# Kernel optimization log

Hardware: AMD Instinct MI355X
Metric: run time of the kernel (lower is better)

## Reference

```python
import math
import jax, jax.numpy as jnp
import numpy as np

NUM_FREQ = 10  # NeRF-style L=10 -> enc dim 3 + 3*2*10 = 63

def pos_encode(coords):
    # freq_bands = 2^i * pi, i = 0..L-1
    freq = (2.0 ** jnp.arange(NUM_FREQ, dtype=coords.dtype)) * math.pi
    scaled = coords[..., None] * freq                      # [E, 3, L]
    enc = jnp.stack([jnp.sin(scaled), jnp.cos(scaled)], axis=-1)  # [E, 3, L, 2]
    enc = enc.reshape(coords.shape[0], -1)                 # [E, 60] interleaved sin/cos
    return jnp.concatenate([coords, enc], axis=-1)         # [E, 63]

def setup_inputs() -> dict:
    key = jax.random.key(0)
    ks = jax.random.split(key, 9)
    N, M, K, C = 65536, 16384, 32, 64
    E = M * K
    x = jax.random.normal(ks[0], (N, C), jnp.float32)
    pos = jax.random.normal(ks[1], (N, 3), jnp.float32)
    batch = jnp.sort(jax.random.randint(ks[2], (N,), 0, 8))
    idx = jax.random.randint(ks[3], (M,), 0, N)
    row = jnp.sort(jax.random.randint(ks[4], (E,), 0, M))
    col = jax.random.randint(ks[5], (E,), 0, N)
    d_in = C + 3 + 3 * 2 * NUM_FREQ  # 127
    def lin(k, i, o):
        s = 1.0 / np.sqrt(i)
        kw, kb = jax.random.split(k)
        return (jax.random.uniform(kw, (i, o), jnp.float32, -s, s),
                jax.random.uniform(kb, (o,), jnp.float32, -s, s))
    lw1, lb1 = lin(ks[6], d_in, 128)
    lw2, lb2 = lin(ks[7], 128, 128)
    gw, gb = lin(ks[8], 128, 256)
    return dict(x=x, pos=pos, batch=batch, idx=idx, row=row, col=col,
                lw1=lw1, lb1=lb1, lw2=lw2, lb2=lb2, gw=gw, gb=gb)

def reference(x, pos, batch, idx, row, col, lw1, lb1, lw2, lb2, gw, gb):
    M = idx.shape[0]
    pos_idx = pos[idx]                         # [M, 3] sampled centers
    pos_diff = pos[col] - pos_idx[row]         # [E, 3] neighbor offsets
    pe = pos_encode(pos_diff)                  # [E, 63]
    edge_in = jnp.concatenate([x[col], pe], axis=-1)   # [E, 127]
    # local_nn: Linear->ReLU->Linear (no final activation, per MLP_Wrapper)
    h = jax.nn.relu(edge_in @ lw1 + lb1)       # [E, 128]
    edge_feat = h @ lw2 + lb2                  # [E, 128]
    # scatter_reduce amax, include_self=False: empty rows stay 0
    agg = jax.ops.segment_max(edge_feat, row, num_segments=M)
    agg = jnp.where(jnp.isneginf(agg), jnp.zeros((), agg.dtype), agg)
    out = agg @ gw + gb                        # [M, 256] global_nn (single Linear)
    return out, pos_idx, batch[idx]
```

## Files before the change

kernel.cpp:

```cpp
#include <hip/hip_runtime.h>
#include <math.h>

#define NN 65536
#define MM 16384
#define EE 524288
#define CF 64
#define HD 128
#define OD 256
#define RPB 8
#define PITCH 129

typedef __bf16 bf16x8 __attribute__((ext_vector_type(8)));
typedef __bf16 bf16x4 __attribute__((ext_vector_type(4)));
typedef float f32x4 __attribute__((ext_vector_type(4)));

__device__ __forceinline__ unsigned enc_f(float f) {
    unsigned u = __float_as_uint(f);
    return (u & 0x80000000u) ? ~u : (u | 0x80000000u);
}
__device__ __forceinline__ float dec_f(unsigned e) {
    unsigned u = (e & 0x80000000u) ? (e ^ 0x80000000u) : ~e;
    return __uint_as_float(u);
}
#define ENC_NEG_INF 0x007FFFFFu

__device__ __forceinline__ unsigned bf_bits(float f) {
    __bf16 b = (__bf16)f;
    return (unsigned)__builtin_bit_cast(unsigned short, b);
}

#define WS_FRAG_OFF 0
#define WS_ROWPTR_OFF 65536
#define WS_XBF_OFF 131072
#define WS_PD_OFF (131072 + 8388608)

__global__ void k_pre(__bf16* __restrict__ fragbuf, int* __restrict__ rowptr,
                      __bf16* __restrict__ xbf, float4* __restrict__ pdbuf,
                      const float* __restrict__ lw1, const float* __restrict__ lw2,
                      const float* __restrict__ x, const int* __restrict__ row,
                      const int* __restrict__ col,
                      const float* __restrict__ pos, const int* __restrict__ batch,
                      const int* __restrict__ idx, float* __restrict__ out) {
    const int b = blockIdx.x;
    const int t = threadIdx.x;
    if (b == 0) {
        const int lane = t & 63;
        const int wv = t >> 6;
        const int q = lane >> 4;
        const int ln = lane & 15;
        #pragma unroll
        for (int fi = 0; fi < 16; ++fi) {
            const int nt = (fi >> 2) & 1, kk = fi & 3;
            const int n = wv * 32 + nt * 16 + ln;
            bf16x8 f;
            #pragma unroll
            for (int j = 0; j < 8; ++j) {
                const int c = kk * 32 + q * 8 + j;
                const int rk = (c < 67) ? c : c - 1;
                f[j] = (fi < 8) ? (__bf16)((c == 67) ? 0.0f : lw1[rk * HD + n])
                                : (__bf16)lw2[c * HD + n];
            }
            *(bf16x8*)&fragbuf[((size_t)fi * 256 + t) * 8] = f;
        }
    } else if (b <= 65) {
        const int i = (b - 1) * 256 + t;
        if (i <= MM) {
            int lo = 0, hi = EE;
            while (lo < hi) { int mid = (lo + hi) >> 1; if (row[mid] < i) lo = mid + 1; else hi = mid; }
            rowptr[i] = lo;
        }
    } else if (b <= 129) {
        const int m = (b - 66) * 256 + t;
        if (m < MM) {
            const int s = idx[m];
            out[MM * OD + m * 3 + 0] = pos[s * 3 + 0];
            out[MM * OD + m * 3 + 1] = pos[s * 3 + 1];
            out[MM * OD + m * 3 + 2] = pos[s * 3 + 2];
            out[MM * OD + MM * 3 + m] = (float)batch[s];
        }
    } else if (b <= 1153) {
        const size_t base = ((size_t)(b - 130) * 256 + t) * 16;
        const float4* xs = (const float4*)(x + base);
        const float4 a = xs[0], c = xs[1], d = xs[2], e = xs[3];
        bf16x8 o0, o1;
        o0[0] = (__bf16)a.x; o0[1] = (__bf16)a.y; o0[2] = (__bf16)a.z; o0[3] = (__bf16)a.w;
        o0[4] = (__bf16)c.x; o0[5] = (__bf16)c.y; o0[6] = (__bf16)c.z; o0[7] = (__bf16)c.w;
        o1[0] = (__bf16)d.x; o1[1] = (__bf16)d.y; o1[2] = (__bf16)d.z; o1[3] = (__bf16)d.w;
        o1[4] = (__bf16)e.x; o1[5] = (__bf16)e.y; o1[6] = (__bf16)e.z; o1[7] = (__bf16)e.w;
        *(bf16x8*)&xbf[base] = o0;
        *(bf16x8*)&xbf[base + 8] = o1;
    } else {
        const int e = (b - 1154) * 256 + t;
        const int r = row[e];
        const int c = col[e];
        const int s = idx[r];
        float4 pd;
        pd.x = pos[c * 3 + 0] - pos[s * 3 + 0];
        pd.y = pos[c * 3 + 1] - pos[s * 3 + 1];
        pd.z = pos[c * 3 + 2] - pos[s * 3 + 2];
        pd.w = 0.0f;
        pdbuf[e] = pd;
    }
}

__launch_bounds__(256)
__global__ void k_fused(const __bf16* __restrict__ xbf, const float4* __restrict__ pdbuf,
                        const int* __restrict__ row, const int* __restrict__ col,
                        const int* __restrict__ rowptr, const __bf16* __restrict__ fragbuf,
                        const float* __restrict__ lb1, const float* __restrict__ lb2,
                        const float* __restrict__ gw, const float* __restrict__ gb,
                        float* __restrict__ out) {
    __shared__ __align__(16) __bf16 einX[64][64];
    __shared__ __align__(16) __bf16 einP[64][64];
    __shared__ __align__(16) __bf16 hbuf[64][HD];
    __shared__ unsigned maxbuf[(RPB + 1) * PITCH];
    __shared__ int srow[2][64];
    const int t = threadIdx.x;
    const int lane = t & 63;
    const int wv = t >> 6;
    const int q = lane >> 4;
    const int ln = lane & 15;
    const int lsw = ln & 7;
    const int m0 = blockIdx.x * RPB;

    const int es = rowptr[m0];
    const int ee = rowptr[m0 + RPB];
    const int ntiles = (ee - es + 63) >> 6;

    for (int i = t; i < (RPB + 1) * PITCH; i += 256) maxbuf[i] = ENC_NEG_INF;

    const int pe_e = t >> 2, pe_part = t & 3, pe_esw = pe_e & 7;
    bf16x8 s0, s1;
    auto issue = [&](int tt) {
        const int eg = min(es + tt * 64 + pe_e, EE - 1);
        const int c = col[eg];
        const bf16x8* xr = (const bf16x8*)(xbf + (size_t)c * CF) + pe_part * 2;
        s0 = xr[0]; s1 = xr[1];
    };
    auto commit = [&]() {
        *(bf16x8*)&einX[pe_e][((pe_part * 2 + 0) ^ pe_esw) * 8] = s0;
        *(bf16x8*)&einX[pe_e][((pe_part * 2 + 1) ^ pe_esw) * 8] = s1;
    };
    auto do_pe = [&](int tt) {
        if (t < 192) {
            const int e = t & 63, d = t >> 6;
            const int sb = tt & 1;
            const int eidx = es + tt * 64 + e;
            const int eg = min(eidx, EE - 1);
            const int esw = e & 7;
            const float4 P = pdbuf[eg];
            const float pd = (d == 0) ? P.x : ((d == 1) ? P.y : P.z);
            if (d == 0) {
                srow[sb][e] = (eidx < ee) ? (row[eg] - m0) : RPB;
                uint2 pkt;
                pkt.x = bf_bits(P.x) | (bf_bits(P.y) << 16);
                pkt.y = bf_bits(P.z);
                *(uint2*)&einP[e][esw * 8] = pkt;
            }
            const float fr = __builtin_amdgcn_fractf(pd * 0.5f);
            float sv = __builtin_amdgcn_sinf(fr);
            float cv = __builtin_amdgcn_cosf(fr);
            #pragma unroll
            for (int l = 0; l < 10; ++l) {
                const int jP = 4 + d * 20 + l * 2;
                *(unsigned*)&einP[e][((jP >> 3) ^ esw) * 8 + (jP & 7)] =
                    bf_bits(sv) | (bf_bits(cv) << 16);
                const float s2 = 2.0f * sv * cv;
                const float c2 = 1.0f - 2.0f * sv * sv;
                sv = s2; cv = c2;
            }
        }
    };

    bf16x8 w1f[2][4];
    #pragma unroll
    for (int nt = 0; nt < 2; ++nt)
        #pragma unroll
        for (int kk = 0; kk < 4; ++kk)
            w1f[nt][kk] = *(const bf16x8*)&fragbuf[((size_t)(nt * 4 + kk) * 256 + t) * 8];
    float4 b1q[2];
    #pragma unroll
    for (int nt = 0; nt < 2; ++nt)
        b1q[nt] = *(const float4*)&lb1[wv * 32 + nt * 16 + q * 4];

    if (ntiles > 0) {
        issue(0);
        commit();
        do_pe(0);
        if (ntiles > 1) issue(1);
    }
    __syncthreads();

    for (int tt = 0; tt < ntiles; ++tt) {
        f32x4 acc[2][4];
        #pragma unroll
        for (int nt = 0; nt < 2; ++nt)
            #pragma unroll
            for (int et = 0; et < 4; ++et)
                acc[nt][et] = (f32x4){b1q[nt].x, b1q[nt].y, b1q[nt].z, b1q[nt].w};
        #pragma unroll
        for (int et = 0; et < 4; ++et) {
            const int e = et * 16 + ln;
            bf16x8 a[4];
            a[0] = *(const bf16x8*)&einX[e][(q ^ lsw) * 8];
            a[1] = *(const bf16x8*)&einX[e][((4 + q) ^ lsw) * 8];
            a[2] = *(const bf16x8*)&einP[e][(q ^ lsw) * 8];
            a[3] = *(const bf16x8*)&einP[e][((4 + q) ^ lsw) * 8];
            #pragma unroll
            for (int kk = 0; kk < 4; ++kk) {
                acc[0][et] = __builtin_amdgcn_mfma_f32_16x16x32_bf16(w1f[0][kk], a[kk], acc[0][et], 0, 0, 0);
                acc[1][et] = __builtin_amdgcn_mfma_f32_16x16x32_bf16(w1f[1][kk], a[kk], acc[1][et], 0, 0, 0);
            }
        }
        #pragma unroll
        for (int et = 0; et < 4; ++et) {
            const int e = et * 16 + ln;
            #pragma unroll
            for (int nt = 0; nt < 2; ++nt) {
                bf16x4 hv;
                hv[0] = (__bf16)fmaxf(acc[nt][et][0], 0.0f);
                hv[1] = (__bf16)fmaxf(acc[nt][et][1], 0.0f);
                hv[2] = (__bf16)fmaxf(acc[nt][et][2], 0.0f);
                hv[3] = (__bf16)fmaxf(acc[nt][et][3], 0.0f);
                const int chunk = wv * 4 + nt * 2 + (q >> 1);
                *(bf16x4*)&hbuf[e][((chunk ^ lsw) * 8) + (q & 1) * 4] = hv;
            }
        }
        __syncthreads();

        {
            if (tt + 1 < ntiles) { commit(); issue(tt + 2 < ntiles ? tt + 2 : tt + 1); }
            bf16x8 w2f[2][4];
            #pragma unroll
            for (int nt = 0; nt < 2; ++nt)
                #pragma unroll
                for (int kk = 0; kk < 4; ++kk)
                    w2f[nt][kk] = *(const bf16x8*)&fragbuf[((size_t)(8 + nt * 4 + kk) * 256 + t) * 8];

            f32x4 acc2[4][2];
            #pragma unroll
            for (int nt = 0; nt < 2; ++nt) {
                const float b2 = lb2[wv * 32 + nt * 16 + ln];
                #pragma unroll
                for (int et = 0; et < 4; ++et)
                    acc2[et][nt] = (f32x4){b2, b2, b2, b2};
            }
            #pragma unroll
            for (int et = 0; et < 4; ++et) {
                const int e = et * 16 + ln;
                #pragma unroll
                for (int kk = 0; kk < 4; ++kk) {
                    bf16x8 ah = *(const bf16x8*)&hbuf[e][((kk * 4 + q) ^ lsw) * 8];
                    acc2[et][0] = __builtin_amdgcn_mfma_f32_16x16x32_bf16(ah, w2f[0][kk], acc2[et][0], 0, 0, 0);
                    acc2[et][1] = __builtin_amdgcn_mfma_f32_16x16x32_bf16(ah, w2f[1][kk], acc2[et][1], 0, 0, 0);
                }
            }
            if (tt + 1 < ntiles) do_pe(tt + 1);
            const int sb = tt & 1;
            #pragma unroll
            for (int et = 0; et < 4; ++et) {
                const int4 R = *(const int4*)&srow[sb][et * 16 + q * 4];
                #pragma unroll
                for (int nt = 0; nt < 2; ++nt) {
                    unsigned* base = maxbuf + (wv * 32 + nt * 16 + ln);
                    const f32x4 vv = acc2[et][nt];
                    int cur = R.x;
                    float m = vv[0];
                    if (R.y != cur) { atomicMax(base + cur * PITCH, enc_f(m)); cur = R.y; m = vv[1]; }
                    else m = fmaxf(m, vv[1]);
                    if (R.z != cur) { atomicMax(base + cur * PITCH, enc_f(m)); cur = R.z; m = vv[2]; }
                    else m = fmaxf(m, vv[2]);
                    if (R.w != cur) { atomicMax(base + cur * PITCH, enc_f(m)); cur = R.w; m = vv[3]; }
                    else m = fmaxf(m, vv[3]);
                    atomicMax(base + cur * PITCH, enc_f(m));
                }
            }
        }
        __syncthreads();
    }

    float* afin = (float*)hbuf;
    for (int i = t; i < RPB * HD; i += 256) {
        const unsigned e = maxbuf[(i >> 7) * PITCH + (i & 127)];
        afin[i] = (e == ENC_NEG_INF) ? 0.0f : dec_f(e);
    }
    __syncthreads();

    const int j4 = (t & 63) * 4;
    const int rbase = (t >> 6) * 2;
    float facc[2][4];
    const float4 bias = *(const float4*)&gb[j4];
    #pragma unroll
    for (int r = 0; r < 2; ++r) { facc[r][0] = bias.x; facc[r][1] = bias.y; facc[r][2] = bias.z; facc[r][3] = bias.w; }
    for (int k = 0; k < 128; k += 4) {
        float4 w0 = *(const float4*)&gw[(k + 0) * OD + j4];
        float4 w1 = *(const float4*)&gw[(k + 1) * OD + j4];
        float4 w2 = *(const float4*)&gw[(k + 2) * OD + j4];
        float4 w3 = *(const float4*)&gw[(k + 3) * OD + j4];
        #pragma unroll
        for (int r = 0; r < 2; ++r) {
            float4 av = *(const float4*)&afin[(rbase + r) * HD + k];
            facc[r][0] += av.x * w0.x + av.y * w1.x + av.z * w2.x + av.w * w3.x;
            facc[r][1] += av.x * w0.y + av.y * w1.y + av.z * w2.y + av.w * w3.y;
            facc[r][2] += av.x * w0.z + av.y * w1.z + av.z * w2.z + av.w * w3.z;
            facc[r][3] += av.x * w0.w + av.y * w1.w + av.z * w2.w + av.w * w3.w;
        }
    }
    #pragma unroll
    for (int r = 0; r < 2; ++r) {
        float4 v; v.x = facc[r][0]; v.y = facc[r][1]; v.z = facc[r][2]; v.w = facc[r][3];
        *(float4*)&out[(size_t)(m0 + rbase + r) * OD + j4] = v;
    }
}

extern "C" void kernel_launch(void* const* d_in, const int* in_sizes, int n_in,
                              void* d_out, int out_size, void* d_ws, size_t ws_size,
                              hipStream_t stream) {
    const float* x   = (const float*)d_in[0];
    const float* pos = (const float*)d_in[1];
    const int* batch = (const int*)d_in[2];
    const int* idx   = (const int*)d_in[3];
    const int* row   = (const int*)d_in[4];
    const int* col   = (const int*)d_in[5];
    const float* lw1 = (const float*)d_in[6];
    const float* lb1 = (const float*)d_in[7];
    const float* lw2 = (const float*)d_in[8];
    const float* lb2 = (const float*)d_in[9];
    const float* gw  = (const float*)d_in[10];
    const float* gb  = (const float*)d_in[11];
    float* out = (float*)d_out;
    __bf16* fragbuf = (__bf16*)((char*)d_ws + WS_FRAG_OFF);
    int* rowptr     = (int*)((char*)d_ws + WS_ROWPTR_OFF);
    __bf16* xbf     = (__bf16*)((char*)d_ws + WS_XBF_OFF);
    float4* pdbuf   = (float4*)((char*)d_ws + WS_PD_OFF);

    hipLaunchKernelGGL(k_pre, dim3(1 + 65 + 64 + 1024 + 2048), dim3(256), 0, stream,
                       fragbuf, rowptr, xbf, pdbuf, lw1, lw2, x, row, col, pos, batch, idx, out);
    hipLaunchKernelGGL(k_fused, dim3(MM / RPB), dim3(256), 0, stream,
                       xbf, pdbuf, row, col, rowptr, fragbuf, lb1, lb2, gw, gb, out);
}
```

Measured before the change: 118.8 us.

## Double edge tile and block size, stream MLP weights per k-slice

Each block now handles 16 output rows and tiles of 128 edges using 512 threads (8 waves). The two halves of the waves each own 64 edges of the tile. The W1/W2 MFMA fragments are no longer held in registers for the whole kernel; they are reloaded from global (L2) per k-slice inside the tile loop, which lowers register pressure to target higher occupancy under launch_bounds(512,4). The intent is to amortize per-block setup, the maxbuf init and the final linear layer over more rows, and to hide latency better. In exchange it adds repeated weight fetches each tile, and the larger shared-memory footprint may cap how many blocks fit per CU.

```diff
diff --git a/kernel.cpp b/kernel.cpp
--- a/kernel.cpp
+++ b/kernel.cpp
@@ -7,7 +7,9 @@
 #define CF 64
 #define HD 128
 #define OD 256
-#define RPB 8
+#define RPB 16
+#define ET 128
+#define BT 512
 #define PITCH 129
 
 typedef __bf16 bf16x8 __attribute__((ext_vector_type(8)));
@@ -103,36 +105,39 @@
     }
 }
 
-__launch_bounds__(256)
+__launch_bounds__(BT, 4)
 __global__ void k_fused(const __bf16* __restrict__ xbf, const float4* __restrict__ pdbuf,
                         const int* __restrict__ row, const int* __restrict__ col,
                         const int* __restrict__ rowptr, const __bf16* __restrict__ fragbuf,
                         const float* __restrict__ lb1, const float* __restrict__ lb2,
                         const float* __restrict__ gw, const float* __restrict__ gb,
                         float* __restrict__ out) {
-    __shared__ __align__(16) __bf16 einX[64][64];
-    __shared__ __align__(16) __bf16 einP[64][64];
-    __shared__ __align__(16) __bf16 hbuf[64][HD];
+    __shared__ __align__(16) __bf16 einX[ET][64];
+    __shared__ __align__(16) __bf16 einP[ET][64];
+    __shared__ __align__(16) __bf16 hbuf[ET][HD];
     __shared__ unsigned maxbuf[(RPB + 1) * PITCH];
-    __shared__ int srow[2][64];
+    __shared__ int srow[2][ET];
     const int t = threadIdx.x;
     const int lane = t & 63;
-    const int wv = t >> 6;
+    const int wv4 = t >> 6;
+    const int hh = wv4 >> 2;
+    const int wv = wv4 & 3;
     const int q = lane >> 4;
     const int ln = lane & 15;
     const int lsw = ln & 7;
+    const int fu = wv * 64 + lane;
     const int m0 = blockIdx.x * RPB;
 
     const int es = rowptr[m0];
     const int ee = rowptr[m0 + RPB];
-    const int ntiles = (ee - es + 63) >> 6;
-
-    for (int i = t; i < (RPB + 1) * PITCH; i += 256) maxbuf[i] = ENC_NEG_INF;
+    const int ntiles = (ee - es + ET - 1) >> 7;
+
+    for (int i = t; i < (RPB + 1) * PITCH; i += BT) maxbuf[i] = ENC_NEG_INF;
 
     const int pe_e = t >> 2, pe_part = t & 3, pe_esw = pe_e & 7;
     bf16x8 s0, s1;
     auto issue = [&](int tt) {
-        const int eg = min(es + tt * 64 + pe_e, EE - 1);
+        const int eg = min(es + tt * ET + pe_e, EE - 1);
         const int c = col[eg];
         const bf16x8* xr = (const bf16x8*)(xbf + (size_t)c * CF) + pe_part * 2;
         s0 = xr[0]; s1 = xr[1];
@@ -142,10 +147,10 @@
         *(bf16x8*)&einX[pe_e][((pe_part * 2 + 1) ^ pe_esw) * 8] = s1;
     };
     auto do_pe = [&](int tt) {
-        if (t < 192) {
-            const int e = t & 63, d = t >> 6;
+        if (t < 384) {
+            const int e = t & 127, d = t >> 7;
             const int sb = tt & 1;
-            const int eidx = es + tt * 64 + e;
+            const int eidx = es + tt * ET + e;
             const int eg = min(eidx, EE - 1);
             const int esw = e & 7;
             const float4 P = pdbuf[eg];
@@ -172,12 +177,6 @@
         }
     };
 
-    bf16x8 w1f[2][4];
-    #pragma unroll
-    for (int nt = 0; nt < 2; ++nt)
-        #pragma unroll
-        for (int kk = 0; kk < 4; ++kk)
-            w1f[nt][kk] = *(const bf16x8*)&fragbuf[((size_t)(nt * 4 + kk) * 256 + t) * 8];
     float4 b1q[2];
     #pragma unroll
     for (int nt = 0; nt < 2; ++nt)
@@ -192,51 +191,46 @@
     __syncthreads();
 
     for (int tt = 0; tt < ntiles; ++tt) {
-        f32x4 acc[2][4];
-        #pragma unroll
-        for (int nt = 0; nt < 2; ++nt)
-            #pragma unroll
-            for (int et = 0; et < 4; ++et)
-                acc[nt][et] = (f32x4){b1q[nt].x, b1q[nt].y, b1q[nt].z, b1q[nt].w};
-        #pragma unroll
-        for (int et = 0; et < 4; ++et) {
-            const int e = et * 16 + ln;
-            bf16x8 a[4];
-            a[0] = *(const bf16x8*)&einX[e][(q ^ lsw) * 8];
-            a[1] = *(const bf16x8*)&einX[e][((4 + q) ^ lsw) * 8];
-            a[2] = *(const bf16x8*)&einP[e][(q ^ lsw) * 8];
-            a[3] = *(const bf16x8*)&einP[e][((4 + q) ^ lsw) * 8];
+        {
+            f32x4 acc[2][4];
+            #pragma unroll
+            for (int nt = 0; nt < 2; ++nt)
+                #pragma unroll
+                for (int et = 0; et < 4; ++et)
+                    acc[nt][et] = (f32x4){b1q[nt].x, b1q[nt].y, b1q[nt].z, b1q[nt].w};
             #pragma unroll
             for (int kk = 0; kk < 4; ++kk) {
-                acc[0][et] = __builtin_amdgcn_mfma_f32_16x16x32_bf16(w1f[0][kk], a[kk], acc[0][et], 0, 0, 0);
-                acc[1][et] = __builtin_amdgcn_mfma_f32_16x16x32_bf16(w1f[1][kk], a[kk], acc[1][et], 0, 0, 0);
-            }
-        }
-        #pragma unroll
-        for (int et = 0; et < 4; ++et) {
-            const int e = et * 16 + ln;
-            #pragma unroll
-            for (int nt = 0; nt < 2; ++nt) {
-                bf16x4 hv;
-                hv[0] = (__bf16)fmaxf(acc[nt][et][0], 0.0f);
-                hv[1] = (__bf16)fmaxf(acc[nt][et][1], 0.0f);
-                hv[2] = (__bf16)fmaxf(acc[nt][et][2], 0.0f);
-                hv[3] = (__bf16)fmaxf(acc[nt][et][3], 0.0f);
-                const int chunk = wv * 4 + nt * 2 + (q >> 1);
-                *(bf16x4*)&hbuf[e][((chunk ^ lsw) * 8) + (q & 1) * 4] = hv;
+                bf16x8 w1a = *(const bf16x8*)&fragbuf[((size_t)(0 * 4 + kk) * 256 + fu) * 8];
+                bf16x8 w1b = *(const bf16x8*)&fragbuf[((size_t)(1 * 4 + kk) * 256 + fu) * 8];
+                #pragma unroll
+                for (int et = 0; et < 4; ++et) {
+                    const int e = hh * 64 + et * 16 + ln;
+                    bf16x8 a = (kk < 2)
+                        ? *(const bf16x8*)&einX[e][((kk * 4 + q) ^ lsw) * 8]
+                        : *(const bf16x8*)&einP[e][(((kk - 2) * 4 + q) ^ lsw) * 8];
+                    acc[0][et] = __builtin_amdgcn_mfma_f32_16x16x32_bf16(w1a, a, acc[0][et], 0, 0, 0);
+                    acc[1][et] = __builtin_amdgcn_mfma_f32_16x16x32_bf16(w1b, a, acc[1][et], 0, 0, 0);
+                }
+            }
+            #pragma unroll
+            for (int et = 0; et < 4; ++et) {
+                const int e = hh * 64 + et * 16 + ln;
+                #pragma unroll
+                for (int nt = 0; nt < 2; ++nt) {
+                    bf16x4 hv;
+                    hv[0] = (__bf16)fmaxf(acc[nt][et][0], 0.0f);
+                    hv[1] = (__bf16)fmaxf(acc[nt][et][1], 0.0f);
+                    hv[2] = (__bf16)fmaxf(acc[nt][et][2], 0.0f);
+                    hv[3] = (__bf16)fmaxf(acc[nt][et][3], 0.0f);
+                    const int chunk = wv * 4 + nt * 2 + (q >> 1);
+                    *(bf16x4*)&hbuf[e][((chunk ^ lsw) * 8) + (q & 1) * 4] = hv;
+                }
             }
         }
         __syncthreads();
 
         {
             if (tt + 1 < ntiles) { commit(); issue(tt + 2 < ntiles ? tt + 2 : tt + 1); }
-            bf16x8 w2f[2][4];
-            #pragma unroll
-            for (int nt = 0; nt < 2; ++nt)
-                #pragma unroll
-                for (int kk = 0; kk < 4; ++kk)
-                    w2f[nt][kk] = *(const bf16x8*)&fragbuf[((size_t)(8 + nt * 4 + kk) * 256 + t) * 8];
-
             f32x4 acc2[4][2];
             #pragma unroll
             for (int nt = 0; nt < 2; ++nt) {
@@ -246,20 +240,22 @@
                     acc2[et][nt] = (f32x4){b2, b2, b2, b2};
             }
             #pragma unroll
-            for (int et = 0; et < 4; ++et) {
-                const int e = et * 16 + ln;
-                #pragma unroll
-                for (int kk = 0; kk < 4; ++kk) {
+            for (int kk = 0; kk < 4; ++kk) {
+                bf16x8 w2a = *(const bf16x8*)&fragbuf[((size_t)(8 + 0 * 4 + kk) * 256 + fu) * 8];
+                bf16x8 w2b = *(const bf16x8*)&fragbuf[((size_t)(8 + 1 * 4 + kk) * 256 + fu) * 8];
+                #pragma unroll
+                for (int et = 0; et < 4; ++et) {
+                    const int e = hh * 64 + et * 16 + ln;
                     bf16x8 ah = *(const bf16x8*)&hbuf[e][((kk * 4 + q) ^ lsw) * 8];
-                    acc2[et][0] = __builtin_amdgcn_mfma_f32_16x16x32_bf16(ah, w2f[0][kk], acc2[et][0], 0, 0, 0);
-                    acc2[et][1] = __builtin_amdgcn_mfma_f32_16x16x32_bf16(ah, w2f[1][kk], acc2[et][1], 0, 0, 0);
+                    acc2[et][0] = __builtin_amdgcn_mfma_f32_16x16x32_bf16(ah, w2a, acc2[et][0], 0, 0, 0);
+                    acc2[et][1] = __builtin_amdgcn_mfma_f32_16x16x32_bf16(ah, w2b, acc2[et][1], 0, 0, 0);
                 }
             }
             if (tt + 1 < ntiles) do_pe(tt + 1);
             const int sb = tt & 1;
             #pragma unroll
             for (int et = 0; et < 4; ++et) {
-                const int4 R = *(const int4*)&srow[sb][et * 16 + q * 4];
+                const int4 R = *(const int4*)&srow[sb][hh * 64 + et * 16 + q * 4];
                 #pragma unroll
                 for (int nt = 0; nt < 2; ++nt) {
                     unsigned* base = maxbuf + (wv * 32 + nt * 16 + ln);
@@ -280,7 +276,7 @@
     }
 
     float* afin = (float*)hbuf;
-    for (int i = t; i < RPB * HD; i += 256) {
+    for (int i = t; i < RPB * HD; i += BT) {
         const unsigned e = maxbuf[(i >> 7) * PITCH + (i & 127)];
         afin[i] = (e == ENC_NEG_INF) ? 0.0f : dec_f(e);
     }
@@ -336,6 +332,6 @@
 
     hipLaunchKernelGGL(k_pre, dim3(1 + 65 + 64 + 1024 + 2048), dim3(256), 0, stream,
                        fragbuf, rowptr, xbf, pdbuf, lw1, lw2, x, row, col, pos, batch, idx, out);
-    hipLaunchKernelGGL(k_fused, dim3(MM / RPB), dim3(256), 0, stream,
+    hipLaunchKernelGGL(k_fused, dim3(MM / RPB), dim3(BT), 0, stream,
                        xbf, pdbuf, row, col, rowptr, fragbuf, lb1, lb2, gw, gb, out);
 }
```

Measured after the change: 166.4 us. +40.1%, slower.
